# Optimization experiments

Measured on AMD Instinct MI355X. Metric: run time of the kernel, lower is better.

## Reference

```python
import jax, jax.numpy as jnp
import numpy as np

GS = 32  # grid_size
TWO_PI = 2.0 * np.pi
DN = ('NCHW', 'OIHW', 'NCHW')


def _circ_conv(x, w, b, pad):
    # PyTorch Conv2d with padding_mode='circular': wrap-pad both spatial dims, then VALID conv.
    if pad > 0:
        x = jnp.pad(x, ((0, 0), (0, 0), (pad, pad), (pad, pad)), mode='wrap')
    y = jax.lax.conv_general_dilated(x, w, (1, 1), 'VALID', dimension_numbers=DN)
    return y + b[None, :, None, None]


def setup_inputs() -> dict:
    key = jax.random.key(0)
    ks = jax.random.split(key, 8)
    B, NN, C, H, W = 4, 20, 128, 8, 32
    return {
        'bbox': jax.random.uniform(ks[0], (B, 4), dtype=jnp.float32),
        'near_locs': jax.random.uniform(ks[1], (B, NN, 2), dtype=jnp.float32),
        'near_feats': jax.random.normal(ks[2], (B, NN, C, H, W), dtype=jnp.float32),
        'overhead_feat': jax.random.normal(ks[3], (B, C, GS, GS), dtype=jnp.float32),
        'rays': jax.random.normal(ks[4], (360, 3, H, W), dtype=jnp.float32),
        'conv1_w': jax.random.normal(ks[5], (1, 8, 3, 3), dtype=jnp.float32) * 0.1,
        'conv1_b': jnp.zeros((1,), jnp.float32),
        'conv2_w': jax.random.normal(ks[6], (1, 8, 5, 5), dtype=jnp.float32) * 0.1,
        'conv2_b': jnp.zeros((1,), jnp.float32),
        'final_w': jax.random.normal(ks[7], (1, 2, 1, 1), dtype=jnp.float32) * 0.1,
        'final_b': jnp.zeros((1,), jnp.float32),
    }


def reference(bbox, near_locs, near_feats, overhead_feat, rays,
              conv1_w, conv1_b, conv2_w, conv2_b, final_w, final_b):
    H, W = rays.shape[-2:]
    L = GS * GS  # num grid locations

    def one(bbox_i, locs_i, feats_i, over_i):
        NN = locs_i.shape[0]
        # ---- grid_helper: distances and bearings from grid cells to neighbors ----
        ys = jnp.linspace(bbox_i[0], bbox_i[2], GS)
        xs = jnp.linspace(bbox_i[1], bbox_i[3], GS)
        gy, gx = jnp.meshgrid(ys, xs, indexing='ij')
        pts = jnp.stack([gy.ravel(), gx.ravel()], axis=-1)          # [L,2]
        d = pts[:, None, :] - locs_i[None, :, :]                    # [L,NN,2]
        D = jnp.sqrt(jnp.sum(d * d, axis=-1) + 1e-12)               # [L,NN]
        theta = jnp.mod(jnp.arctan2(d[..., 1], d[..., 0]), TWO_PI)  # [L,NN] in [0,2pi)
        # ---- ray gather by rounded degree ----
        inds = jnp.mod(jnp.round(jnp.rad2deg(theta)).astype(jnp.int32), 360)
        orientation = rays[inds]                                    # [L,NN,3,H,W]
        distance = jnp.broadcast_to(D[:, :, None, None, None], (L, NN, 1, H, W))
        # ---- panorama channels: per-neighbor max/mean over feature dim ----
        pano = jnp.stack([feats_i.max(axis=1), feats_i.mean(axis=1)], axis=1)  # [NN,2,H,W]
        x_pano = jnp.broadcast_to(pano[None], (L, NN, 2, H, W))
        # ---- overhead channels: per-grid-cell max/mean over channel dim ----
        over_flat = over_i.reshape(over_i.shape[0], -1).T           # [L,C]
        ov = jnp.stack([over_flat.max(axis=1), over_flat.mean(axis=1)], axis=1)  # [L,2]
        x_over = jnp.broadcast_to(ov[:, :, None, None][:, None], (L, NN, 2, H, W))
        # ---- concat geo features, run small circular convs + 1x1 fusion ----
        inp = jnp.concatenate([distance, orientation, x_pano, x_over], axis=2)  # [L,NN,8,H,W]
        inp = inp.reshape(L * NN, inp.shape[2], H, W)
        c1 = _circ_conv(inp, conv1_w, conv1_b, 1)
        c2 = _circ_conv(inp, conv2_w, conv2_b, 2)
        fused = jnp.concatenate([c1, c2], axis=1)                   # [L*NN,2,H,W]
        logits = _circ_conv(fused, final_w, final_b, 0)             # [L*NN,1,H,W]
        logits = logits.reshape(L, NN, H, W)
        # ---- softmax over (NN,H,W) per grid cell, weighted aggregation ----
        w = jax.nn.softmax(logits.reshape(L, -1), axis=-1).reshape(L, NN, H, W)
        grid_feats = jnp.einsum('pfxy,spxy->sf', feats_i, w).reshape(GS, GS, -1)
        attn = w.reshape(GS, GS, NN, H, W)
        return grid_feats, attn

    return jax.vmap(one)(bbox, near_locs, near_feats, overhead_feat)
```

## Files before the change

kernel.cpp:

```cpp
#include <hip/hip_runtime.h>

#define B_  4
#define NN_ 20
#define C_  128
#define H_  8
#define W_  32
#define P_  256
#define GS_ 32
#define L_  1024
#define K_  5120


__global__ __launch_bounds__(256) void k_front(const float* __restrict__ feats,
                                               const float* __restrict__ rays,
                                               const float* __restrict__ bbox,
                                               const float* __restrict__ locs,
                                               const float* __restrict__ w1,
                                               const float* __restrict__ w2,
                                               const float* __restrict__ b1,
                                               const float* __restrict__ b2,
                                               const float* __restrict__ fw,
                                               const float* __restrict__ fb,
                                               float* __restrict__ Rc,
                                               float* __restrict__ eRc,
                                               float* __restrict__ Pc,
                                               float* __restrict__ ePc,
                                               int* __restrict__ ind,
                                               float* __restrict__ Kscal,
                                               float* __restrict__ Ft) {
  __shared__ float s[32 * 257];
  int bid = blockIdx.x, tid = threadIdx.x;
  if (bid < 360) {
    int a = bid;
    #pragma unroll
    for (int c = 0; c < 3; ++c) s[c * P_ + tid] = rays[(a * 3 + c) * P_ + tid];
    __syncthreads();
    int y = tid >> 5, x = tid & 31;
    float acc1 = 0.f, acc2 = 0.f;
    #pragma unroll
    for (int c = 0; c < 3; ++c) {
      const float* sc  = s + c * P_;
      const float* w1c = w1 + (1 + c) * 9;
      const float* w2c = w2 + (1 + c) * 25;
      #pragma unroll
      for (int dy = 0; dy < 3; ++dy) { int yy = ((y + dy + 7) & 7) * 32;
        #pragma unroll
        for (int dx = 0; dx < 3; ++dx) { int xx = (x + dx + 31) & 31;
          acc1 += sc[yy + xx] * w1c[dy * 3 + dx]; } }
      #pragma unroll
      for (int dy = 0; dy < 5; ++dy) { int yy = ((y + dy + 6) & 7) * 32;
        #pragma unroll
        for (int dx = 0; dx < 5; ++dx) { int xx = (x + dx + 30) & 31;
          acc2 += sc[yy + xx] * w2c[dy * 5 + dx]; } }
    }
    float v = fw[0] * acc1 + fw[1] * acc2;
    Rc[a * P_ + tid]  = v;
    eRc[a * P_ + tid] = expf(v);
  } else if (bid < 440) {
    int bn = bid - 360;
    const float* src = feats + bn * C_ * P_ + tid;
    float mx = -3.4e38f, sm = 0.f;
    #pragma unroll 8
    for (int c = 0; c < C_; ++c) { float v = src[c * P_]; mx = fmaxf(mx, v); sm += v; }
    s[tid]      = mx;
    s[P_ + tid] = sm * (1.0f / 128.0f);
    __syncthreads();
    int y = tid >> 5, x = tid & 31;
    float acc1 = 0.f, acc2 = 0.f;
    #pragma unroll
    for (int c = 0; c < 2; ++c) {
      const float* sc  = s + c * P_;
      const float* w1c = w1 + (4 + c) * 9;
      const float* w2c = w2 + (4 + c) * 25;
      #pragma unroll
      for (int dy = 0; dy < 3; ++dy) { int yy = ((y + dy + 7) & 7) * 32;
        #pragma unroll
        for (int dx = 0; dx < 3; ++dx) { int xx = (x + dx + 31) & 31;
          acc1 += sc[yy + xx] * w1c[dy * 3 + dx]; } }
      #pragma unroll
      for (int dy = 0; dy < 5; ++dy) { int yy = ((y + dy + 6) & 7) * 32;
        #pragma unroll
        for (int dx = 0; dx < 5; ++dx) { int xx = (x + dx + 30) & 31;
          acc2 += sc[yy + xx] * w2c[dy * 5 + dx]; } }
    }
    float v = fw[0] * acc1 + fw[1] * acc2;
    Pc[bn * P_ + tid]  = v;
    ePc[bn * P_ + tid] = expf(v);
  } else if (bid < 760) {
    int t = (bid - 440) * 256 + tid;
    int n = t % NN_;
    int r = t / NN_;
    int l = r & 1023, b = r >> 10;
    int i = l >> 5, j = l & 31;
    float y0 = bbox[b * 4 + 0], x0 = bbox[b * 4 + 1];
    float y1 = bbox[b * 4 + 2], x1 = bbox[b * 4 + 3];
    float gy = (i == 31) ? y1 : (y0 + ((y1 - y0) / 31.0f) * (float)i);
    float gx = (j == 31) ? x1 : (x0 + ((x1 - x0) / 31.0f) * (float)j);
    float d0 = gy - locs[(b * NN_ + n) * 2 + 0];
    float d1 = gx - locs[(b * NN_ + n) * 2 + 1];
    float D  = sqrtf(d0 * d0 + d1 * d1 + 1e-12f);
    float th = atan2f(d1, d0);
    if (th < 0.f) th += 6.283185307179586f;
    float deg = th * 57.29577951308232f;
    int di = (int)rintf(deg);
    if (di >= 360) di -= 360;
    float s10 = 0.f, s20 = 0.f;
    #pragma unroll
    for (int q = 0; q < 9; ++q) s10 += w1[q];
    #pragma unroll
    for (int q = 0; q < 25; ++q) s20 += w2[q];
    ind[t]   = di;
    Kscal[t] = fw[0] * (D * s10 + b1[0]) + fw[1] * (D * s20 + b2[0]) + fb[0];
  } else {
    int bb = bid - 760;
    int bn = bb >> 2, cq = bb & 3;
    int b = bn / NN_, n = bn % NN_;
    int c0 = cq * 32;
    #pragma unroll 4
    for (int cc = 0; cc < 32; ++cc)
      s[cc * 257 + tid] = feats[(bn * C_ + c0 + cc) * P_ + tid];
    __syncthreads();
    int c = tid & 31, p8 = tid >> 5;
    #pragma unroll 4
    for (int pp = 0; pp < 32; ++pp) {
      int p = pp * 8 + p8;
      Ft[((size_t)b * K_ + n * P_ + p) * C_ + c0 + c] = s[c * 257 + p];
    }
  }
}

__global__ __launch_bounds__(256) void k_G(const float* __restrict__ eRc,
                                           const float* __restrict__ ePc,
                                           const float* __restrict__ Ft,
                                           float* __restrict__ G) {
  __shared__ __align__(16) float sW[128 * 36];
  int bid = blockIdx.x;
  int at = bid % 12;
  int n  = (bid / 12) % NN_;
  int b  = bid / 240;
  int a0 = at << 5;
  int tid = threadIdx.x;
  int w8 = (tid >> 6) << 3;
  int lane = tid & 63;
  int q  = lane >> 4;
  int c0 = (lane & 15) << 2;
  int kst = tid & 127, hst = tid >> 7;
  float4 aL[8], aH[8];
  #pragma unroll
  for (int r = 0; r < 8; ++r) {
    aL[r] = make_float4(0.f, 0.f, 0.f, 0.f);
    aH[r] = make_float4(0.f, 0.f, 0.f, 0.f);
  }
  const float* epc   = ePc + (b * NN_ + n) * P_;
  const float* fbase = Ft + ((size_t)(b * NN_ + n) * P_ + q) * C_ + c0;
  for (int pc0 = 0; pc0 < 256; pc0 += 128) {
    __syncthreads();
    #pragma unroll
    for (int r = 0; r < 16; ++r) {
      int ar = a0 + hst * 16 + r;
      if (ar > 359) ar = 359;
      sW[kst * 36 + hst * 16 + r] = eRc[ar * P_ + pc0 + kst] * epc[pc0 + kst];
    }
    __syncthreads();
    const float* fp  = fbase + (size_t)pc0 * C_;
    const float* swk = sW + q * 36 + w8;
#define FMA8(r, wgt, f0, f1) \
    aL[r].x += (wgt) * f0.x; aL[r].y += (wgt) * f0.y; \
    aL[r].z += (wgt) * f0.z; aL[r].w += (wgt) * f0.w; \
    aH[r].x += (wgt) * f1.x; aH[r].y += (wgt) * f1.y; \
    aH[r].z += (wgt) * f1.z; aH[r].w += (wgt) * f1.w;
#define FMA64(wa, wb, f0, f1) \
    FMA8(0, wa.x, f0, f1) FMA8(1, wa.y, f0, f1) FMA8(2, wa.z, f0, f1) \
    FMA8(3, wa.w, f0, f1) FMA8(4, wb.x, f0, f1) FMA8(5, wb.y, f0, f1) \
    FMA8(6, wb.z, f0, f1) FMA8(7, wb.w, f0, f1)
    float4 fa0 = *(const float4*)(fp);
    float4 fb0 = *(const float4*)(fp + 64);
    #pragma unroll
    for (int kk = 0; kk < 128; kk += 8) {
      float4 fa1 = *(const float4*)(fp + (size_t)(kk + 4) * C_);
      float4 fb1 = *(const float4*)(fp + (size_t)(kk + 4) * C_ + 64);
      float4 wa  = *(const float4*)(swk + kk * 36);
      float4 wb  = *(const float4*)(swk + kk * 36 + 4);
      FMA64(wa, wb, fa0, fb0)
      int pk = (kk + 8 < 128) ? (kk + 8) : 0;
      fa0 = *(const float4*)(fp + (size_t)pk * C_);
      fb0 = *(const float4*)(fp + (size_t)pk * C_ + 64);
      wa  = *(const float4*)(swk + (kk + 4) * 36);
      wb  = *(const float4*)(swk + (kk + 4) * 36 + 4);
      FMA64(wa, wb, fa1, fb1)
    }
#undef FMA64
#undef FMA8
  }
#define RED2(v) { v += __shfl_xor(v, 16); v += __shfl_xor(v, 32); }
  #pragma unroll
  for (int r = 0; r < 8; ++r) {
    RED2(aL[r].x) RED2(aL[r].y) RED2(aL[r].z) RED2(aL[r].w)
    RED2(aH[r].x) RED2(aH[r].y) RED2(aH[r].z) RED2(aH[r].w)
  }
#undef RED2
  #pragma unroll
  for (int r = 0; r < 8; ++r) {
    if ((r >> 1) == q) {
      int a = a0 + w8 + r;
      if (a < 360) {
        float* pt = G + (((size_t)b * 360 + a) * NN_ + n) * C_;
        *(float4*)(pt + c0)      = aL[r];
        *(float4*)(pt + c0 + 64) = aH[r];
      }
    }
  }
}

__global__ __launch_bounds__(256) void k_soft(const float* __restrict__ Rc,
                                              const float* __restrict__ Pc,
                                              const float* __restrict__ Kscal,
                                              const int* __restrict__ ind,
                                              const float* __restrict__ G,
                                              float* __restrict__ attn,
                                              float* __restrict__ gf) {
  int bl = blockIdx.x;
  int b = bl >> 10;
  int tid = threadIdx.x;
  __shared__ float sK[NN_];
  __shared__ int   sI[NN_];
  __shared__ float red[8];
  if (tid < NN_) { sI[tid] = ind[bl * NN_ + tid]; sK[tid] = Kscal[bl * NN_ + tid]; }
  __syncthreads();
  float lg[NN_];
  #pragma unroll
  for (int n = 0; n < NN_; ++n)
    lg[n] = Rc[sI[n] * P_ + tid] + Pc[(b * NN_ + n) * P_ + tid] + sK[n];
  float m = -3.4e38f;
  #pragma unroll
  for (int n = 0; n < NN_; ++n) m = fmaxf(m, lg[n]);
  #pragma unroll
  for (int off = 32; off > 0; off >>= 1) m = fmaxf(m, __shfl_xor(m, off));
  if ((tid & 63) == 0) red[tid >> 6] = m;
  __syncthreads();
  m = fmaxf(fmaxf(red[0], red[1]), fmaxf(red[2], red[3]));
  float ssum = 0.f;
  #pragma unroll
  for (int n = 0; n < NN_; ++n) { lg[n] = expf(lg[n] - m); ssum += lg[n]; }
  #pragma unroll
  for (int off = 32; off > 0; off >>= 1) ssum += __shfl_xor(ssum, off);
  if ((tid & 63) == 0) red[4 + (tid >> 6)] = ssum;
  __syncthreads();
  float inv = 1.0f / ((red[4] + red[5]) + (red[6] + red[7]));
  #pragma unroll
  for (int n = 0; n < NN_; ++n)
    attn[((size_t)bl * NN_ + n) * P_ + tid] = lg[n] * inv;
  if (tid < C_) {
    float acc = 0.f;
    #pragma unroll
    for (int n = 0; n < NN_; ++n) {
      float wn = expf(sK[n] - m) * inv;
      acc += wn * G[(((size_t)b * 360 + sI[n]) * NN_ + n) * C_ + tid];
    }
    gf[(size_t)bl * C_ + tid] = acc;
  }
}

extern "C" void kernel_launch(void* const* d_in, const int* in_sizes, int n_in,
                              void* d_out, int out_size, void* d_ws, size_t ws_size,
                              hipStream_t stream) {
  const float* bbox  = (const float*)d_in[0];
  const float* locs  = (const float*)d_in[1];
  const float* feats = (const float*)d_in[2];
  const float* rays  = (const float*)d_in[4];
  const float* w1    = (const float*)d_in[5];
  const float* b1    = (const float*)d_in[6];
  const float* w2    = (const float*)d_in[7];
  const float* b2    = (const float*)d_in[8];
  const float* fw    = (const float*)d_in[9];
  const float* fb    = (const float*)d_in[10];

  float* ws     = (float*)d_ws;
  int*   ind    = (int*)ws;
  float* Kscal  = ws + 81920;
  float* Rc     = ws + 163840;
  float* Pc     = ws + 256000;
  float* ePc    = ws + 276480;
  float* Ft     = ws + 325632;
  float* G      = ws + 2947072;
  float* eRc    = ws + 6633472;

  float* gf   = (float*)d_out;
  float* attn = gf + (B_ * L_ * C_);

  k_front<<<1080, 256, 0, stream>>>(feats, rays, bbox, locs, w1, w2, b1, b2,
                                    fw, fb, Rc, eRc, Pc, ePc, ind, Kscal, Ft);
  k_G    <<<960, 256, 0, stream>>>(eRc, ePc, Ft, G);
  k_soft <<<4096, 256, 0, stream>>>(Rc, Pc, Kscal, ind, G, attn, gf);
}
```

Before: 172.4 us.

## Precompute softmax normalizers in k_G to drop per-cell max/sum reductions

The logits factor into exp(Rc)*exp(Pc)*exp(K), so k_G now also sums the eRc*ePc products per (angle, neighbor) into S. k_soft then builds each cell's partition function from 20 scalar lookups instead of reading full logits and doing block-wide max and sum reductions. Attention is written directly as a product of the precomputed exponentials. This removes the Rc/Pc buffers and two reduction barriers, but drops max-subtraction, so large logits could overflow.

```diff
diff --git a/kernel.cpp b/kernel.cpp
--- a/kernel.cpp
+++ b/kernel.cpp
@@ -21,9 +21,7 @@
                                                const float* __restrict__ b2,
                                                const float* __restrict__ fw,
                                                const float* __restrict__ fb,
-                                               float* __restrict__ Rc,
                                                float* __restrict__ eRc,
-                                               float* __restrict__ Pc,
                                                float* __restrict__ ePc,
                                                int* __restrict__ ind,
                                                float* __restrict__ Kscal,
@@ -53,9 +51,7 @@
         for (int dx = 0; dx < 5; ++dx) { int xx = (x + dx + 30) & 31;
           acc2 += sc[yy + xx] * w2c[dy * 5 + dx]; } }
     }
-    float v = fw[0] * acc1 + fw[1] * acc2;
-    Rc[a * P_ + tid]  = v;
-    eRc[a * P_ + tid] = expf(v);
+    eRc[a * P_ + tid] = expf(fw[0] * acc1 + fw[1] * acc2);
   } else if (bid < 440) {
     int bn = bid - 360;
     const float* src = feats + bn * C_ * P_ + tid;
@@ -83,9 +79,7 @@
         for (int dx = 0; dx < 5; ++dx) { int xx = (x + dx + 30) & 31;
           acc2 += sc[yy + xx] * w2c[dy * 5 + dx]; } }
     }
-    float v = fw[0] * acc1 + fw[1] * acc2;
-    Pc[bn * P_ + tid]  = v;
-    ePc[bn * P_ + tid] = expf(v);
+    ePc[bn * P_ + tid] = expf(fw[0] * acc1 + fw[1] * acc2);
   } else if (bid < 760) {
     int t = (bid - 440) * 256 + tid;
     int n = t % NN_;
@@ -132,7 +126,8 @@
 __global__ __launch_bounds__(256) void k_G(const float* __restrict__ eRc,
                                            const float* __restrict__ ePc,
                                            const float* __restrict__ Ft,
-                                           float* __restrict__ G) {
+                                           float* __restrict__ G,
+                                           float* __restrict__ S) {
   __shared__ __align__(16) float sW[128 * 36];
   int bid = blockIdx.x;
   int at = bid % 12;
@@ -151,6 +146,7 @@
     aL[r] = make_float4(0.f, 0.f, 0.f, 0.f);
     aH[r] = make_float4(0.f, 0.f, 0.f, 0.f);
   }
+  float sS = 0.f;
   const float* epc   = ePc + (b * NN_ + n) * P_;
   const float* fbase = Ft + ((size_t)(b * NN_ + n) * P_ + q) * C_ + c0;
   for (int pc0 = 0; pc0 < 256; pc0 += 128) {
@@ -162,6 +158,12 @@
       sW[kst * 36 + hst * 16 + r] = eRc[ar * P_ + pc0 + kst] * epc[pc0 + kst];
     }
     __syncthreads();
+    if (tid < 32) {
+      float t = 0.f;
+      #pragma unroll 8
+      for (int p = 0; p < 128; ++p) t += sW[p * 36 + tid];
+      sS += t;
+    }
     const float* fp  = fbase + (size_t)pc0 * C_;
     const float* swk = sW + q * 36 + w8;
 #define FMA8(r, wgt, f0, f1) \
@@ -210,53 +212,49 @@
       }
     }
   }
-}
-
-__global__ __launch_bounds__(256) void k_soft(const float* __restrict__ Rc,
-                                              const float* __restrict__ Pc,
+  if (tid < 32) {
+    int a = a0 + tid;
+    if (a < 360) S[((size_t)b * 360 + a) * NN_ + n] = sS;
+  }
+}
+
+__global__ __launch_bounds__(256) void k_soft(const float* __restrict__ eRc,
+                                              const float* __restrict__ ePc,
                                               const float* __restrict__ Kscal,
                                               const int* __restrict__ ind,
+                                              const float* __restrict__ S,
                                               const float* __restrict__ G,
                                               float* __restrict__ attn,
                                               float* __restrict__ gf) {
   int bl = blockIdx.x;
   int b = bl >> 10;
   int tid = threadIdx.x;
-  __shared__ float sK[NN_];
+  __shared__ float sE[NN_];
   __shared__ int   sI[NN_];
-  __shared__ float red[8];
-  if (tid < NN_) { sI[tid] = ind[bl * NN_ + tid]; sK[tid] = Kscal[bl * NN_ + tid]; }
+  __shared__ float sZ[NN_];
+  if (tid < NN_) {
+    int i = ind[bl * NN_ + tid];
+    float ek = expf(Kscal[bl * NN_ + tid]);
+    sI[tid] = i;
+    sE[tid] = ek;
+    sZ[tid] = ek * S[((size_t)b * 360 + i) * NN_ + tid];
+  }
   __syncthreads();
-  float lg[NN_];
-  #pragma unroll
-  for (int n = 0; n < NN_; ++n)
-    lg[n] = Rc[sI[n] * P_ + tid] + Pc[(b * NN_ + n) * P_ + tid] + sK[n];
-  float m = -3.4e38f;
-  #pragma unroll
-  for (int n = 0; n < NN_; ++n) m = fmaxf(m, lg[n]);
-  #pragma unroll
-  for (int off = 32; off > 0; off >>= 1) m = fmaxf(m, __shfl_xor(m, off));
-  if ((tid & 63) == 0) red[tid >> 6] = m;
-  __syncthreads();
-  m = fmaxf(fmaxf(red[0], red[1]), fmaxf(red[2], red[3]));
-  float ssum = 0.f;
-  #pragma unroll
-  for (int n = 0; n < NN_; ++n) { lg[n] = expf(lg[n] - m); ssum += lg[n]; }
-  #pragma unroll
-  for (int off = 32; off > 0; off >>= 1) ssum += __shfl_xor(ssum, off);
-  if ((tid & 63) == 0) red[4 + (tid >> 6)] = ssum;
-  __syncthreads();
-  float inv = 1.0f / ((red[4] + red[5]) + (red[6] + red[7]));
-  #pragma unroll
-  for (int n = 0; n < NN_; ++n)
-    attn[((size_t)bl * NN_ + n) * P_ + tid] = lg[n] * inv;
+  float Z = 0.f;
+  #pragma unroll
+  for (int n = 0; n < NN_; ++n) Z += sZ[n];
+  float invZ = 1.0f / Z;
+  #pragma unroll
+  for (int n = 0; n < NN_; ++n) {
+    float wn = sE[n] * invZ;
+    attn[((size_t)bl * NN_ + n) * P_ + tid] =
+        wn * eRc[sI[n] * P_ + tid] * ePc[(b * NN_ + n) * P_ + tid];
+  }
   if (tid < C_) {
     float acc = 0.f;
     #pragma unroll
-    for (int n = 0; n < NN_; ++n) {
-      float wn = expf(sK[n] - m) * inv;
-      acc += wn * G[(((size_t)b * 360 + sI[n]) * NN_ + n) * C_ + tid];
-    }
+    for (int n = 0; n < NN_; ++n)
+      acc += (sE[n] * invZ) * G[(((size_t)b * 360 + sI[n]) * NN_ + n) * C_ + tid];
     gf[(size_t)bl * C_ + tid] = acc;
   }
 }
@@ -278,18 +276,17 @@
   float* ws     = (float*)d_ws;
   int*   ind    = (int*)ws;
   float* Kscal  = ws + 81920;
-  float* Rc     = ws + 163840;
-  float* Pc     = ws + 256000;
-  float* ePc    = ws + 276480;
+  float* eRc    = ws + 163840;
+  float* ePc    = ws + 256000;
+  float* S      = ws + 276480;
   float* Ft     = ws + 325632;
   float* G      = ws + 2947072;
-  float* eRc    = ws + 6633472;
 
   float* gf   = (float*)d_out;
   float* attn = gf + (B_ * L_ * C_);
 
   k_front<<<1080, 256, 0, stream>>>(feats, rays, bbox, locs, w1, w2, b1, b2,
-                                    fw, fb, Rc, eRc, Pc, ePc, ind, Kscal, Ft);
-  k_G    <<<960, 256, 0, stream>>>(eRc, ePc, Ft, G);
-  k_soft <<<4096, 256, 0, stream>>>(Rc, Pc, Kscal, ind, G, attn, gf);
-}
+                                    fw, fb, eRc, ePc, ind, Kscal, Ft);
+  k_G    <<<960, 256, 0, stream>>>(eRc, ePc, Ft, G, S);
+  k_soft <<<4096, 256, 0, stream>>>(eRc, ePc, Kscal, ind, S, G, attn, gf);
+}
```

After: 167.3 us. 1.03x faster.
